# Optimization experiments

Hardware: AMD Instinct MI355X
Metric: run time of the kernel (lower is better)

The kernel has to match this reference:

```python
import jax, jax.numpy as jnp
import numpy as np

EPS_MI = 1e-9
EPS_BN = 1e-5


def conv_bn_relu(x, W, b, g, beta, rm, rv):
    # 1x1 conv as channel contraction; eval-mode BatchNorm; ReLU.
    y = jnp.einsum('oc,bchw->bohw', W, x) + b[None, :, None, None]
    y = (y - rm[None, :, None, None]) / jnp.sqrt(rv[None, :, None, None] + EPS_BN)
    y = y * g[None, :, None, None] + beta[None, :, None, None]
    return jax.nn.relu(y)


def linear(x, W, b):
    return x @ W.T + b


def compute_entropy(feat):
    B, C, H, W = feat.shape
    p = jax.nn.softmax(feat.reshape(B, C, H * W), axis=2)  # [B,C,N]
    return -jnp.sum(p * jnp.log(p + EPS_MI), axis=2)        # [B,C]


def compute_mutual_information(vis_feat, text_feat):
    B, C, H, W = vis_feat.shape
    N = H * W
    vn = jax.nn.softmax(vis_feat.reshape(B, C, N), axis=2)   # [B,C,N]
    tn = jax.nn.softmax(text_feat.reshape(B, C, N), axis=2)  # [B,C,N]
    joint = vn[:, :, :, None] * tn[:, :, None, :]            # [B,C,N,N]
    joint = joint / jnp.sum(joint, axis=(2, 3), keepdims=True)
    p_v = jnp.sum(vn, axis=2)                                # [B,C]
    p_t = jnp.sum(tn, axis=2)                                # [B,C]
    denom = (p_v * p_t + EPS_MI)[:, :, None, None]
    mi = jnp.sum(joint * jnp.log(joint / denom + EPS_MI), axis=(2, 3))
    return mi                                                # [B,C]


def setup_inputs() -> dict:
    key = jax.random.key(0)
    ks = jax.random.split(key, 16)
    B, C, H, W = 8, 256, 16, 16
    s = 0.05
    inp = {
        'vis_feat': jax.random.normal(ks[0], (B, C, H, W), jnp.float32),
        'text_feat': jax.random.normal(ks[1], (B, C, H, W), jnp.float32),
        # transform: Conv2d(C,C,1) + BN
        'Wt': jax.random.normal(ks[2], (C, C), jnp.float32) * s,
        'bt': jnp.zeros((C,), jnp.float32),
        'g1': jnp.ones((C,), jnp.float32),
        'b1': jnp.zeros((C,), jnp.float32),
        'm1': jnp.zeros((C,), jnp.float32),
        'v1': jnp.ones((C,), jnp.float32),
        # entropy_weight MLP: Linear(2C,C) -> ReLU -> Linear(C,C) -> Sigmoid
        'We1': jax.random.normal(ks[3], (C, 2 * C), jnp.float32) * s,
        'be1': jnp.zeros((C,), jnp.float32),
        'We2': jax.random.normal(ks[4], (C, C), jnp.float32) * s,
        'be2': jnp.zeros((C,), jnp.float32),
        # mi_weight MLP: Linear(C,C) -> ReLU -> Linear(C,C) -> Sigmoid
        'Wm1': jax.random.normal(ks[5], (C, C), jnp.float32) * s,
        'bm1': jnp.zeros((C,), jnp.float32),
        'Wm2': jax.random.normal(ks[6], (C, C), jnp.float32) * s,
        'bm2': jnp.zeros((C,), jnp.float32),
        # fusion: Conv2d(2C,C,1) + BN
        'Wf': jax.random.normal(ks[7], (C, 2 * C), jnp.float32) * s,
        'bf': jnp.zeros((C,), jnp.float32),
        'g2': jnp.ones((C,), jnp.float32),
        'b2': jnp.zeros((C,), jnp.float32),
        'm2': jnp.zeros((C,), jnp.float32),
        'v2': jnp.ones((C,), jnp.float32),
    }
    return inp


def reference(vis_feat, text_feat, Wt, bt, g1, b1, m1, v1,
              We1, be1, We2, be2, Wm1, bm1, Wm2, bm2,
              Wf, bf, g2, b2, m2, v2):
    B, C, H, W = vis_feat.shape
    vis_trans = conv_bn_relu(vis_feat, Wt, bt, g1, b1, m1, v1)
    text_trans = conv_bn_relu(text_feat, Wt, bt, g1, b1, m1, v1)

    vis_entropy = compute_entropy(vis_trans)
    text_entropy = compute_entropy(text_trans)
    entropy_concat = jnp.concatenate([vis_entropy, text_entropy], axis=1)  # [B,2C]
    ew = jax.nn.sigmoid(linear(jax.nn.relu(linear(entropy_concat, We1, be1)), We2, be2))

    mi = compute_mutual_information(vis_trans, text_trans)
    mw = jax.nn.sigmoid(linear(jax.nn.relu(linear(mi, Wm1, bm1)), Wm2, bm2))

    ew = ew[:, :, None, None]
    mw = mw[:, :, None, None]
    weighted_vis = vis_trans * ew * mw
    weighted_text = text_trans * (1.0 - ew) * mw
    fused = conv_bn_relu(jnp.concatenate([weighted_vis, weighted_text], axis=1),
                         Wf, bf, g2, b2, m2, v2)
    return fused
```

## Files before the change

kernel.cpp:

```cpp
#include <hip/hip_runtime.h>
#include <hip/hip_bf16.h>

__device__ __forceinline__ float relu_keepnan(float a) { return a < 0.f ? 0.f : a; }

__global__ void __launch_bounds__(256) k_transform(
    const float* __restrict__ vis,
    const float* __restrict__ text,
    const float* __restrict__ Wt,
    const float* __restrict__ bt,
    const float* __restrict__ g1,
    const float* __restrict__ b1,
    const float* __restrict__ m1,
    const float* __restrict__ v1,
    __hip_bfloat16* __restrict__ ws_trans,
    float* __restrict__ ws_ent)
{
    const int m = blockIdx.x;
    const int obase = blockIdx.y * 8;
    const int tid = threadIdx.x;

    __shared__ float Yl[8][256];

    const float* x = (m < 8) ? (vis + m * 65536) : (text + (m - 8) * 65536);
    const float* Wb = Wt + obase * 256;

    float acc[8];
#pragma unroll
    for (int j = 0; j < 8; j++) acc[j] = 0.f;

    float xc[8], xn[8];
#pragma unroll
    for (int i = 0; i < 8; i++) xc[i] = x[i * 256 + tid];

    for (int c0 = 0; c0 < 248; c0 += 8) {
#pragma unroll
        for (int i = 0; i < 8; i++) xn[i] = x[(c0 + 8 + i) * 256 + tid];
#pragma unroll
        for (int j = 0; j < 8; j++) {
#pragma unroll
            for (int i = 0; i < 8; i++) acc[j] += Wb[j * 256 + c0 + i] * xc[i];
        }
#pragma unroll
        for (int i = 0; i < 8; i++) xc[i] = xn[i];
    }
#pragma unroll
    for (int j = 0; j < 8; j++) {
#pragma unroll
        for (int i = 0; i < 8; i++) acc[j] += Wb[j * 256 + 248 + i] * xc[i];
    }

#pragma unroll
    for (int j = 0; j < 8; j++) {
        int o = obase + j;
        float inv = rsqrtf(v1[o] + 1e-5f);
        float sc = g1[o] * inv;
        float bi = (bt[o] - m1[o]) * sc + b1[o];
        float y = relu_keepnan(acc[j] * sc + bi);
        ws_trans[(m * 256 + o) * 256 + tid] = (__hip_bfloat16)y;
        Yl[j][tid] = y;
    }
    __syncthreads();

    const int wave = tid >> 6, lane = tid & 63;
#pragma unroll
    for (int jj = 0; jj < 2; jj++) {
        int row = wave * 2 + jj;
        float a0 = Yl[row][lane];
        float a1 = Yl[row][64 + lane];
        float a2 = Yl[row][128 + lane];
        float a3 = Yl[row][192 + lane];
        float mx = fmaxf(fmaxf(a0, a1), fmaxf(a2, a3));
#pragma unroll
        for (int off = 32; off > 0; off >>= 1) mx = fmaxf(mx, __shfl_xor(mx, off, 64));
        float z0 = a0 - mx, z1 = a1 - mx, z2 = a2 - mx, z3 = a3 - mx;
        float e0 = expf(z0), e1 = expf(z1), e2 = expf(z2), e3 = expf(z3);
        float s = e0 + e1 + e2 + e3;
        float d = z0 * e0 + z1 * e1 + z2 * e2 + z3 * e3;
#pragma unroll
        for (int off = 32; off > 0; off >>= 1) {
            s += __shfl_xor(s, off, 64);
            d += __shfl_xor(d, off, 64);
        }
        if (lane == 0) ws_ent[m * 256 + obase + row] = logf(s) - d / s;
    }
}

__global__ void __launch_bounds__(256) k_mlp1(
    const float* __restrict__ ws_ent,
    const float* __restrict__ We1, const float* __restrict__ be1,
    const float* __restrict__ Wm1, const float* __restrict__ bm1,
    float* __restrict__ h1, float* __restrict__ h2)
{
    const int o = blockIdx.x;
    const int lane = threadIdx.x & 63;
    const int wave = threadIdx.x >> 6;

    float w1[8];
#pragma unroll
    for (int i = 0; i < 8; i++) w1[i] = We1[o * 512 + lane + 64 * i];
    float w2[4];
#pragma unroll
    for (int i = 0; i < 4; i++) w2[i] = Wm1[o * 256 + lane + 64 * i];

#pragma unroll
    for (int bb = 0; bb < 2; bb++) {
        const int b = wave * 2 + bb;
        float ev[4], et[4];
#pragma unroll
        for (int i = 0; i < 4; i++) {
            ev[i] = ws_ent[b * 256 + lane + 64 * i];
            et[i] = ws_ent[(b + 8) * 256 + lane + 64 * i];
        }
        float s = 0.f, t = 0.f;
#pragma unroll
        for (int i = 0; i < 4; i++) {
            s += w1[i] * ev[i] + w1[4 + i] * et[i];
            t += w2[i] * (-(ev[i] + et[i]));
        }
#pragma unroll
        for (int off = 32; off > 0; off >>= 1) {
            s += __shfl_xor(s, off, 64);
            t += __shfl_xor(t, off, 64);
        }
        if (lane == 0) {
            h1[b * 256 + o] = relu_keepnan(be1[o] + s);
            h2[b * 256 + o] = relu_keepnan(bm1[o] + t);
        }
    }
}

__global__ void __launch_bounds__(256) k_mlp2(
    const float* __restrict__ h1, const float* __restrict__ h2,
    const float* __restrict__ We2, const float* __restrict__ be2,
    const float* __restrict__ Wm2, const float* __restrict__ bm2,
    float* __restrict__ ws_sv, float* __restrict__ ws_st)
{
    const int o = blockIdx.x;
    const int lane = threadIdx.x & 63;
    const int wave = threadIdx.x >> 6;

    float w1[4], w2[4];
#pragma unroll
    for (int i = 0; i < 4; i++) {
        w1[i] = We2[o * 256 + lane + 64 * i];
        w2[i] = Wm2[o * 256 + lane + 64 * i];
    }

#pragma unroll
    for (int bb = 0; bb < 2; bb++) {
        const int b = wave * 2 + bb;
        float s = 0.f, t = 0.f;
#pragma unroll
        for (int i = 0; i < 4; i++) {
            s += w1[i] * h1[b * 256 + lane + 64 * i];
            t += w2[i] * h2[b * 256 + lane + 64 * i];
        }
#pragma unroll
        for (int off = 32; off > 0; off >>= 1) {
            s += __shfl_xor(s, off, 64);
            t += __shfl_xor(t, off, 64);
        }
        if (lane == 0) {
            float ew = 1.f / (1.f + expf(-(be2[o] + s)));
            float mw = 1.f / (1.f + expf(-(bm2[o] + t)));
            ws_sv[b * 256 + o] = ew * mw;
            ws_st[b * 256 + o] = (1.f - ew) * mw;
        }
    }
}

__global__ void __launch_bounds__(256) k_fused(
    const __hip_bfloat16* __restrict__ ws_trans,
    const float* __restrict__ ws_sv, const float* __restrict__ ws_st,
    const float* __restrict__ Wf, const float* __restrict__ bfv,
    const float* __restrict__ g2, const float* __restrict__ b2,
    const float* __restrict__ m2, const float* __restrict__ v2,
    float* __restrict__ out)
{
    const int b = blockIdx.x;
    const int obase = blockIdx.y * 4;
    const int tid = threadIdx.x;

    const float* Wb = Wf + obase * 512;

    float acc[4];
#pragma unroll
    for (int j = 0; j < 4; j++) acc[j] = 0.f;

#pragma unroll
    for (int half = 0; half < 2; half++) {
        const __hip_bfloat16* xh = ws_trans + ((half ? 8 + b : b) * 256) * 256;
        const float* gh = (half ? ws_st : ws_sv) + b * 256;
        const float* Wh = Wb + half * 256;

        float xc[8], xn[8];
#pragma unroll
        for (int i = 0; i < 8; i++) xc[i] = (float)xh[i * 256 + tid];

        for (int c0 = 0; c0 < 248; c0 += 8) {
#pragma unroll
            for (int i = 0; i < 8; i++) xn[i] = (float)xh[(c0 + 8 + i) * 256 + tid];
#pragma unroll
            for (int i = 0; i < 8; i++) {
                float xs = xc[i] * gh[c0 + i];
#pragma unroll
                for (int j = 0; j < 4; j++) acc[j] += Wh[j * 512 + c0 + i] * xs;
            }
#pragma unroll
            for (int i = 0; i < 8; i++) xc[i] = xn[i];
        }
#pragma unroll
        for (int i = 0; i < 8; i++) {
            float xs = xc[i] * gh[248 + i];
#pragma unroll
            for (int j = 0; j < 4; j++) acc[j] += Wh[j * 512 + 248 + i] * xs;
        }
    }

#pragma unroll
    for (int j = 0; j < 4; j++) {
        int o = obase + j;
        float inv = rsqrtf(v2[o] + 1e-5f);
        float sc = g2[o] * inv;
        float bi = (bfv[o] - m2[o]) * sc + b2[o];
        float y = relu_keepnan(acc[j] * sc + bi);
        if (y == 0.f) y = 1e-8f;
        out[(b * 256 + o) * 256 + tid] = y;
    }
}

extern "C" void kernel_launch(void* const* d_in, const int* in_sizes, int n_in,
                              void* d_out, int out_size, void* d_ws, size_t ws_size,
                              hipStream_t stream) {
    const float* vis  = (const float*)d_in[0];
    const float* text = (const float*)d_in[1];
    const float* Wt   = (const float*)d_in[2];
    const float* bt   = (const float*)d_in[3];
    const float* g1   = (const float*)d_in[4];
    const float* b1   = (const float*)d_in[5];
    const float* m1   = (const float*)d_in[6];
    const float* v1   = (const float*)d_in[7];
    const float* We1  = (const float*)d_in[8];
    const float* be1  = (const float*)d_in[9];
    const float* We2  = (const float*)d_in[10];
    const float* be2  = (const float*)d_in[11];
    const float* Wm1  = (const float*)d_in[12];
    const float* bm1  = (const float*)d_in[13];
    const float* Wm2  = (const float*)d_in[14];
    const float* bm2  = (const float*)d_in[15];
    const float* Wf   = (const float*)d_in[16];
    const float* bfv  = (const float*)d_in[17];
    const float* g2   = (const float*)d_in[18];
    const float* b2   = (const float*)d_in[19];
    const float* m2   = (const float*)d_in[20];
    const float* v2   = (const float*)d_in[21];
    float* out = (float*)d_out;

    char* ws = (char*)d_ws;
    __hip_bfloat16* ws_trans = (__hip_bfloat16*)ws;
    float* ws_ent = (float*)(ws + 2097152);
    float* ws_sv  = (float*)(ws + 2097152 + 16384);
    float* ws_st  = (float*)(ws + 2097152 + 16384 + 8192);
    float* ws_h1  = (float*)(ws + 2097152 + 16384 + 16384);
    float* ws_h2  = (float*)(ws + 2097152 + 16384 + 24576);

    k_transform<<<dim3(16, 32), 256, 0, stream>>>(vis, text, Wt, bt, g1, b1, m1, v1,
                                                  ws_trans, ws_ent);
    k_mlp1<<<dim3(256), 256, 0, stream>>>(ws_ent, We1, be1, Wm1, bm1, ws_h1, ws_h2);
    k_mlp2<<<dim3(256), 256, 0, stream>>>(ws_h1, ws_h2, We2, be2, Wm2, bm2, ws_sv, ws_st);
    k_fused<<<dim3(8, 64), 256, 0, stream>>>(ws_trans, ws_sv, ws_st, Wf, bfv, g2, b2, m2, v2,
                                             out);
}
```

Baseline: 161.5 us.

## Merge four kernels into one cooperative kernel with grid-wide syncs

Replaces the four separate launches (transform, two MLP stages, fused conv) with a single cooperative kernel of 256 blocks that separates the stages with grid.sync(). Each block now computes 16 output channels in the transform stage and 8 in the final conv, up from 8 and 4, so the work is re-tiled to fit the smaller grid. The aim is to remove per-launch overhead and inter-kernel gaps. In exchange, the grid is smaller (256 blocks versus 512 before), each thread holds more registers, and grid-wide barriers add their own cost.

```diff
diff --git a/kernel.cpp b/kernel.cpp
--- a/kernel.cpp
+++ b/kernel.cpp
@@ -1,231 +1,222 @@
 #include <hip/hip_runtime.h>
 #include <hip/hip_bf16.h>
+#include <hip/hip_cooperative_groups.h>
+
+namespace cg = cooperative_groups;
 
 __device__ __forceinline__ float relu_keepnan(float a) { return a < 0.f ? 0.f : a; }
 
-__global__ void __launch_bounds__(256) k_transform(
-    const float* __restrict__ vis,
-    const float* __restrict__ text,
-    const float* __restrict__ Wt,
-    const float* __restrict__ bt,
-    const float* __restrict__ g1,
-    const float* __restrict__ b1,
-    const float* __restrict__ m1,
-    const float* __restrict__ v1,
-    __hip_bfloat16* __restrict__ ws_trans,
-    float* __restrict__ ws_ent)
-{
-    const int m = blockIdx.x;
-    const int obase = blockIdx.y * 8;
-    const int tid = threadIdx.x;
-
-    __shared__ float Yl[8][256];
-
-    const float* x = (m < 8) ? (vis + m * 65536) : (text + (m - 8) * 65536);
-    const float* Wb = Wt + obase * 256;
-
-    float acc[8];
-#pragma unroll
-    for (int j = 0; j < 8; j++) acc[j] = 0.f;
-
-    float xc[8], xn[8];
-#pragma unroll
-    for (int i = 0; i < 8; i++) xc[i] = x[i * 256 + tid];
-
-    for (int c0 = 0; c0 < 248; c0 += 8) {
-#pragma unroll
-        for (int i = 0; i < 8; i++) xn[i] = x[(c0 + 8 + i) * 256 + tid];
-#pragma unroll
-        for (int j = 0; j < 8; j++) {
-#pragma unroll
-            for (int i = 0; i < 8; i++) acc[j] += Wb[j * 256 + c0 + i] * xc[i];
-        }
-#pragma unroll
-        for (int i = 0; i < 8; i++) xc[i] = xn[i];
-    }
-#pragma unroll
-    for (int j = 0; j < 8; j++) {
-#pragma unroll
-        for (int i = 0; i < 8; i++) acc[j] += Wb[j * 256 + 248 + i] * xc[i];
-    }
-
-#pragma unroll
-    for (int j = 0; j < 8; j++) {
-        int o = obase + j;
-        float inv = rsqrtf(v1[o] + 1e-5f);
-        float sc = g1[o] * inv;
-        float bi = (bt[o] - m1[o]) * sc + b1[o];
-        float y = relu_keepnan(acc[j] * sc + bi);
-        ws_trans[(m * 256 + o) * 256 + tid] = (__hip_bfloat16)y;
-        Yl[j][tid] = y;
-    }
-    __syncthreads();
-
-    const int wave = tid >> 6, lane = tid & 63;
-#pragma unroll
-    for (int jj = 0; jj < 2; jj++) {
-        int row = wave * 2 + jj;
-        float a0 = Yl[row][lane];
-        float a1 = Yl[row][64 + lane];
-        float a2 = Yl[row][128 + lane];
-        float a3 = Yl[row][192 + lane];
-        float mx = fmaxf(fmaxf(a0, a1), fmaxf(a2, a3));
-#pragma unroll
-        for (int off = 32; off > 0; off >>= 1) mx = fmaxf(mx, __shfl_xor(mx, off, 64));
-        float z0 = a0 - mx, z1 = a1 - mx, z2 = a2 - mx, z3 = a3 - mx;
-        float e0 = expf(z0), e1 = expf(z1), e2 = expf(z2), e3 = expf(z3);
-        float s = e0 + e1 + e2 + e3;
-        float d = z0 * e0 + z1 * e1 + z2 * e2 + z3 * e3;
-#pragma unroll
-        for (int off = 32; off > 0; off >>= 1) {
-            s += __shfl_xor(s, off, 64);
-            d += __shfl_xor(d, off, 64);
-        }
-        if (lane == 0) ws_ent[m * 256 + obase + row] = logf(s) - d / s;
-    }
-}
-
-__global__ void __launch_bounds__(256) k_mlp1(
-    const float* __restrict__ ws_ent,
+__global__ void __launch_bounds__(256) k_all(
+    const float* __restrict__ vis, const float* __restrict__ text,
+    const float* __restrict__ Wt, const float* __restrict__ bt,
+    const float* __restrict__ g1, const float* __restrict__ b1,
+    const float* __restrict__ m1, const float* __restrict__ v1,
     const float* __restrict__ We1, const float* __restrict__ be1,
+    const float* __restrict__ We2, const float* __restrict__ be2,
     const float* __restrict__ Wm1, const float* __restrict__ bm1,
-    float* __restrict__ h1, float* __restrict__ h2)
-{
-    const int o = blockIdx.x;
-    const int lane = threadIdx.x & 63;
-    const int wave = threadIdx.x >> 6;
-
-    float w1[8];
-#pragma unroll
-    for (int i = 0; i < 8; i++) w1[i] = We1[o * 512 + lane + 64 * i];
-    float w2[4];
-#pragma unroll
-    for (int i = 0; i < 4; i++) w2[i] = Wm1[o * 256 + lane + 64 * i];
-
-#pragma unroll
-    for (int bb = 0; bb < 2; bb++) {
-        const int b = wave * 2 + bb;
-        float ev[4], et[4];
-#pragma unroll
-        for (int i = 0; i < 4; i++) {
-            ev[i] = ws_ent[b * 256 + lane + 64 * i];
-            et[i] = ws_ent[(b + 8) * 256 + lane + 64 * i];
-        }
-        float s = 0.f, t = 0.f;
-#pragma unroll
-        for (int i = 0; i < 4; i++) {
-            s += w1[i] * ev[i] + w1[4 + i] * et[i];
-            t += w2[i] * (-(ev[i] + et[i]));
-        }
-#pragma unroll
-        for (int off = 32; off > 0; off >>= 1) {
-            s += __shfl_xor(s, off, 64);
-            t += __shfl_xor(t, off, 64);
-        }
-        if (lane == 0) {
-            h1[b * 256 + o] = relu_keepnan(be1[o] + s);
-            h2[b * 256 + o] = relu_keepnan(bm1[o] + t);
-        }
-    }
-}
-
-__global__ void __launch_bounds__(256) k_mlp2(
-    const float* __restrict__ h1, const float* __restrict__ h2,
-    const float* __restrict__ We2, const float* __restrict__ be2,
     const float* __restrict__ Wm2, const float* __restrict__ bm2,
-    float* __restrict__ ws_sv, float* __restrict__ ws_st)
-{
-    const int o = blockIdx.x;
-    const int lane = threadIdx.x & 63;
-    const int wave = threadIdx.x >> 6;
-
-    float w1[4], w2[4];
-#pragma unroll
-    for (int i = 0; i < 4; i++) {
-        w1[i] = We2[o * 256 + lane + 64 * i];
-        w2[i] = Wm2[o * 256 + lane + 64 * i];
-    }
-
-#pragma unroll
-    for (int bb = 0; bb < 2; bb++) {
-        const int b = wave * 2 + bb;
-        float s = 0.f, t = 0.f;
-#pragma unroll
-        for (int i = 0; i < 4; i++) {
-            s += w1[i] * h1[b * 256 + lane + 64 * i];
-            t += w2[i] * h2[b * 256 + lane + 64 * i];
-        }
-#pragma unroll
-        for (int off = 32; off > 0; off >>= 1) {
-            s += __shfl_xor(s, off, 64);
-            t += __shfl_xor(t, off, 64);
-        }
-        if (lane == 0) {
-            float ew = 1.f / (1.f + expf(-(be2[o] + s)));
-            float mw = 1.f / (1.f + expf(-(bm2[o] + t)));
-            ws_sv[b * 256 + o] = ew * mw;
-            ws_st[b * 256 + o] = (1.f - ew) * mw;
-        }
-    }
-}
-
-__global__ void __launch_bounds__(256) k_fused(
-    const __hip_bfloat16* __restrict__ ws_trans,
-    const float* __restrict__ ws_sv, const float* __restrict__ ws_st,
     const float* __restrict__ Wf, const float* __restrict__ bfv,
     const float* __restrict__ g2, const float* __restrict__ b2,
     const float* __restrict__ m2, const float* __restrict__ v2,
+    __hip_bfloat16* __restrict__ ws_trans,
+    float* __restrict__ ws_ent,
+    float* __restrict__ ws_sv, float* __restrict__ ws_st,
+    float* __restrict__ h1, float* __restrict__ h2,
     float* __restrict__ out)
 {
-    const int b = blockIdx.x;
-    const int obase = blockIdx.y * 4;
+    cg::grid_group grid = cg::this_grid();
+    const int blk = blockIdx.x;
     const int tid = threadIdx.x;
-
-    const float* Wb = Wf + obase * 512;
-
-    float acc[4];
-#pragma unroll
-    for (int j = 0; j < 4; j++) acc[j] = 0.f;
-
-#pragma unroll
-    for (int half = 0; half < 2; half++) {
-        const __hip_bfloat16* xh = ws_trans + ((half ? 8 + b : b) * 256) * 256;
-        const float* gh = (half ? ws_st : ws_sv) + b * 256;
-        const float* Wh = Wb + half * 256;
+    const int lane = tid & 63;
+    const int wave = tid >> 6;
+
+    __shared__ float Yl[16][256];
+
+    {
+        const int m = blk >> 4;
+        const int obase = (blk & 15) * 16;
+        const float* x = (m < 8) ? (vis + m * 65536) : (text + (m - 8) * 65536);
+        const float* Wb = Wt + obase * 256;
+
+        float acc[16];
+#pragma unroll
+        for (int j = 0; j < 16; j++) acc[j] = 0.f;
 
         float xc[8], xn[8];
 #pragma unroll
-        for (int i = 0; i < 8; i++) xc[i] = (float)xh[i * 256 + tid];
+        for (int i = 0; i < 8; i++) xc[i] = x[i * 256 + tid];
 
         for (int c0 = 0; c0 < 248; c0 += 8) {
 #pragma unroll
-            for (int i = 0; i < 8; i++) xn[i] = (float)xh[(c0 + 8 + i) * 256 + tid];
+            for (int i = 0; i < 8; i++) xn[i] = x[(c0 + 8 + i) * 256 + tid];
+#pragma unroll
+            for (int j = 0; j < 16; j++) {
+#pragma unroll
+                for (int i = 0; i < 8; i++) acc[j] += Wb[j * 256 + c0 + i] * xc[i];
+            }
+#pragma unroll
+            for (int i = 0; i < 8; i++) xc[i] = xn[i];
+        }
+#pragma unroll
+        for (int j = 0; j < 16; j++) {
+#pragma unroll
+            for (int i = 0; i < 8; i++) acc[j] += Wb[j * 256 + 248 + i] * xc[i];
+        }
+
+#pragma unroll
+        for (int j = 0; j < 16; j++) {
+            int o = obase + j;
+            float inv = rsqrtf(v1[o] + 1e-5f);
+            float sc = g1[o] * inv;
+            float bi = (bt[o] - m1[o]) * sc + b1[o];
+            float y = relu_keepnan(acc[j] * sc + bi);
+            ws_trans[(m * 256 + o) * 256 + tid] = (__hip_bfloat16)y;
+            Yl[j][tid] = y;
+        }
+        __syncthreads();
+
+#pragma unroll
+        for (int jj = 0; jj < 4; jj++) {
+            int row = wave * 4 + jj;
+            float a0 = Yl[row][lane];
+            float a1 = Yl[row][64 + lane];
+            float a2 = Yl[row][128 + lane];
+            float a3 = Yl[row][192 + lane];
+            float mx = fmaxf(fmaxf(a0, a1), fmaxf(a2, a3));
+#pragma unroll
+            for (int off = 32; off > 0; off >>= 1) mx = fmaxf(mx, __shfl_xor(mx, off, 64));
+            float z0 = a0 - mx, z1 = a1 - mx, z2 = a2 - mx, z3 = a3 - mx;
+            float e0 = expf(z0), e1 = expf(z1), e2 = expf(z2), e3 = expf(z3);
+            float s = e0 + e1 + e2 + e3;
+            float d = z0 * e0 + z1 * e1 + z2 * e2 + z3 * e3;
+#pragma unroll
+            for (int off = 32; off > 0; off >>= 1) {
+                s += __shfl_xor(s, off, 64);
+                d += __shfl_xor(d, off, 64);
+            }
+            if (lane == 0) ws_ent[m * 256 + obase + row] = logf(s) - d / s;
+        }
+    }
+    grid.sync();
+
+    {
+        const int o = blk;
+        float w1[8];
+#pragma unroll
+        for (int i = 0; i < 8; i++) w1[i] = We1[o * 512 + lane + 64 * i];
+        float w2[4];
+#pragma unroll
+        for (int i = 0; i < 4; i++) w2[i] = Wm1[o * 256 + lane + 64 * i];
+
+#pragma unroll
+        for (int bb = 0; bb < 2; bb++) {
+            const int b = wave * 2 + bb;
+            float ev[4], et[4];
+#pragma unroll
+            for (int i = 0; i < 4; i++) {
+                ev[i] = ws_ent[b * 256 + lane + 64 * i];
+                et[i] = ws_ent[(b + 8) * 256 + lane + 64 * i];
+            }
+            float s = 0.f, t = 0.f;
+#pragma unroll
+            for (int i = 0; i < 4; i++) {
+                s += w1[i] * ev[i] + w1[4 + i] * et[i];
+                t += w2[i] * (-(ev[i] + et[i]));
+            }
+#pragma unroll
+            for (int off = 32; off > 0; off >>= 1) {
+                s += __shfl_xor(s, off, 64);
+                t += __shfl_xor(t, off, 64);
+            }
+            if (lane == 0) {
+                h1[b * 256 + o] = relu_keepnan(be1[o] + s);
+                h2[b * 256 + o] = relu_keepnan(bm1[o] + t);
+            }
+        }
+    }
+    grid.sync();
+
+    {
+        const int o = blk;
+        float w1[4], w2[4];
+#pragma unroll
+        for (int i = 0; i < 4; i++) {
+            w1[i] = We2[o * 256 + lane + 64 * i];
+            w2[i] = Wm2[o * 256 + lane + 64 * i];
+        }
+#pragma unroll
+        for (int bb = 0; bb < 2; bb++) {
+            const int b = wave * 2 + bb;
+            float s = 0.f, t = 0.f;
+#pragma unroll
+            for (int i = 0; i < 4; i++) {
+                s += w1[i] * h1[b * 256 + lane + 64 * i];
+                t += w2[i] * h2[b * 256 + lane + 64 * i];
+            }
+#pragma unroll
+            for (int off = 32; off > 0; off >>= 1) {
+                s += __shfl_xor(s, off, 64);
+                t += __shfl_xor(t, off, 64);
+            }
+            if (lane == 0) {
+                float ew = 1.f / (1.f + expf(-(be2[o] + s)));
+                float mw = 1.f / (1.f + expf(-(bm2[o] + t)));
+                ws_sv[b * 256 + o] = ew * mw;
+                ws_st[b * 256 + o] = (1.f - ew) * mw;
+            }
+        }
+    }
+    grid.sync();
+
+    {
+        const int b = blk >> 5;
+        const int obase = (blk & 31) * 8;
+        const float* Wb = Wf + obase * 512;
+
+        float acc[8];
+#pragma unroll
+        for (int j = 0; j < 8; j++) acc[j] = 0.f;
+
+#pragma unroll
+        for (int half = 0; half < 2; half++) {
+            const __hip_bfloat16* xh = ws_trans + ((half ? 8 + b : b) * 256) * 256;
+            const float* gh = (half ? ws_st : ws_sv) + b * 256;
+            const float* Wh = Wb + half * 256;
+
+            float xc[8], xn[8];
+#pragma unroll
+            for (int i = 0; i < 8; i++) xc[i] = (float)xh[i * 256 + tid];
+
+            for (int c0 = 0; c0 < 248; c0 += 8) {
+#pragma unroll
+                for (int i = 0; i < 8; i++) xn[i] = (float)xh[(c0 + 8 + i) * 256 + tid];
+#pragma unroll
+                for (int i = 0; i < 8; i++) {
+                    float xs = xc[i] * gh[c0 + i];
+#pragma unroll
+                    for (int j = 0; j < 8; j++) acc[j] += Wh[j * 512 + c0 + i] * xs;
+                }
+#pragma unroll
+                for (int i = 0; i < 8; i++) xc[i] = xn[i];
+            }
 #pragma unroll
             for (int i = 0; i < 8; i++) {
-                float xs = xc[i] * gh[c0 + i];
-#pragma unroll
-                for (int j = 0; j < 4; j++) acc[j] += Wh[j * 512 + c0 + i] * xs;
-            }
-#pragma unroll
-            for (int i = 0; i < 8; i++) xc[i] = xn[i];
-        }
-#pragma unroll
-        for (int i = 0; i < 8; i++) {
-            float xs = xc[i] * gh[248 + i];
-#pragma unroll
-            for (int j = 0; j < 4; j++) acc[j] += Wh[j * 512 + 248 + i] * xs;
-        }
-    }
-
-#pragma unroll
-    for (int j = 0; j < 4; j++) {
-        int o = obase + j;
-        float inv = rsqrtf(v2[o] + 1e-5f);
-        float sc = g2[o] * inv;
-        float bi = (bfv[o] - m2[o]) * sc + b2[o];
-        float y = relu_keepnan(acc[j] * sc + bi);
-        if (y == 0.f) y = 1e-8f;
-        out[(b * 256 + o) * 256 + tid] = y;
+                float xs = xc[i] * gh[248 + i];
+#pragma unroll
+                for (int j = 0; j < 8; j++) acc[j] += Wh[j * 512 + 248 + i] * xs;
+            }
+        }
+
+#pragma unroll
+        for (int j = 0; j < 8; j++) {
+            int o = obase + j;
+            float inv = rsqrtf(v2[o] + 1e-5f);
+            float sc = g2[o] * inv;
+            float bi = (bfv[o] - m2[o]) * sc + b2[o];
+            float y = relu_keepnan(acc[j] * sc + bi);
+            if (y == 0.f) y = 1e-8f;
+            out[(b * 256 + o) * 256 + tid] = y;
+        }
     }
 }
 
@@ -264,10 +255,16 @@
     float* ws_h1  = (float*)(ws + 2097152 + 16384 + 16384);
     float* ws_h2  = (float*)(ws + 2097152 + 16384 + 24576);
 
-    k_transform<<<dim3(16, 32), 256, 0, stream>>>(vis, text, Wt, bt, g1, b1, m1, v1,
-                                                  ws_trans, ws_ent);
-    k_mlp1<<<dim3(256), 256, 0, stream>>>(ws_ent, We1, be1, Wm1, bm1, ws_h1, ws_h2);
-    k_mlp2<<<dim3(256), 256, 0, stream>>>(ws_h1, ws_h2, We2, be2, Wm2, bm2, ws_sv, ws_st);
-    k_fused<<<dim3(8, 64), 256, 0, stream>>>(ws_trans, ws_sv, ws_st, Wf, bfv, g2, b2, m2, v2,
-                                             out);
+    void* args[] = {
+        (void*)&vis, (void*)&text, (void*)&Wt, (void*)&bt,
+        (void*)&g1, (void*)&b1, (void*)&m1, (void*)&v1,
+        (void*)&We1, (void*)&be1, (void*)&We2, (void*)&be2,
+        (void*)&Wm1, (void*)&bm1, (void*)&Wm2, (void*)&bm2,
+        (void*)&Wf, (void*)&bfv, (void*)&g2, (void*)&b2,
+        (void*)&m2, (void*)&v2,
+        (void*)&ws_trans, (void*)&ws_ent, (void*)&ws_sv, (void*)&ws_st,
+        (void*)&ws_h1, (void*)&ws_h2, (void*)&out
+    };
+    hipLaunchCooperativeKernel((const void*)k_all, dim3(256), dim3(256),
+                               args, 0, stream);
 }
```

Result: slower. 290.7 us (+80.0%).
